# Performance work log

Hardware: AMD Instinct MI355X
Metric: run time of the kernel (lower is better)

Reference implementation:

```python
import jax, jax.numpy as jnp
import numpy as np
from jax import lax

DN = ('NCHW', 'OIHW', 'NCHW')
EPS = 1e-5

def conv2d(x, w):
    return lax.conv_general_dilated(x, w, (1, 1), 'VALID', dimension_numbers=DN)

def bn(x, g, b, m, v):
    # eval-mode BatchNorm2d, params shape [C]
    scale = (g / jnp.sqrt(v + EPS))[None, :, None, None]
    shift = (b - m * g / jnp.sqrt(v + EPS))[None, :, None, None]
    return x * scale + shift

def xcorr_depthwise(search, kernel):
    # search [B,C,Hs,Ws], kernel [B,C,hk,wk] -> [B,C,Hs-hk+1,Ws-wk+1]
    B, C, Hs, Ws = search.shape
    hk, wk = kernel.shape[2], kernel.shape[3]
    s = search.reshape(1, B * C, Hs, Ws)
    k = kernel.reshape(B * C, 1, hk, wk)
    out = lax.conv_general_dilated(s, k, (1, 1), 'VALID',
                                   dimension_numbers=DN,
                                   feature_group_count=B * C)
    return out.reshape(B, C, Hs - hk + 1, Ws - wk + 1)

def _bn_params(key, c):
    k1, k2, k3, k4 = jax.random.split(key, 4)
    g = jax.random.uniform(k1, (c,), jnp.float32, 0.5, 1.5)
    b = jax.random.normal(k2, (c,), jnp.float32) * 0.1
    m = jax.random.normal(k3, (c,), jnp.float32) * 0.1
    v = jax.random.uniform(k4, (c,), jnp.float32, 0.5, 1.5)
    return g, b, m, v

def setup_inputs() -> dict:
    key = jax.random.key(0)
    ks = jax.random.split(key, 10)
    IN, H, OUT = 256, 256, 10
    kernel = jax.random.normal(ks[0], (128, IN, 7, 7), jnp.float32)
    search = jax.random.normal(ks[1], (128, IN, 31, 31), jnp.float32)
    w_ck = jax.random.normal(ks[2], (H, IN, 3, 3), jnp.float32) * 0.05
    g1, b1, m1, v1 = _bn_params(ks[3], H)
    w_cs = jax.random.normal(ks[4], (H, IN, 3, 3), jnp.float32) * 0.05
    g2, b2, m2, v2 = _bn_params(ks[5], H)
    w_h1 = jax.random.normal(ks[6], (H, H, 1, 1), jnp.float32) * 0.05
    g3, b3, m3, v3 = _bn_params(ks[7], H)
    w_h2 = jax.random.normal(ks[8], (OUT, H, 1, 1), jnp.float32) * 0.05
    b_h2 = jax.random.normal(ks[9], (OUT,), jnp.float32) * 0.05
    return dict(kernel=kernel, search=search, w_ck=w_ck, g1=g1, b1=b1, m1=m1, v1=v1,
                w_cs=w_cs, g2=g2, b2=b2, m2=m2, v2=v2,
                w_h1=w_h1, g3=g3, b3=b3, m3=m3, v3=v3, w_h2=w_h2, b_h2=b_h2)

def reference(kernel, search, w_ck, g1, b1, m1, v1, w_cs, g2, b2, m2, v2,
              w_h1, g3, b3, m3, v3, w_h2, b_h2):
    # conv_kernel / conv_search branches: Conv3x3 -> BN -> ReLU
    k = jax.nn.relu(bn(conv2d(kernel, w_ck), g1, b1, m1, v1))   # [B,256,5,5]
    s = jax.nn.relu(bn(conv2d(search, w_cs), g2, b2, m2, v2))   # [B,256,29,29]
    # depthwise cross-correlation (search_crop/search_pos are None -> kernel_t = kernel)
    feat = xcorr_depthwise(s, k)                                 # [B,256,25,25]
    # head: Conv1x1 -> BN -> ReLU -> Conv1x1(+bias)
    h = jax.nn.relu(bn(conv2d(feat, w_h1), g3, b3, m3, v3))
    out = conv2d(h, w_h2) + b_h2[None, :, None, None]            # [B,10,25,25]
    return out
```

## Files before the change

kernel.cpp:

```cpp
#include <hip/hip_runtime.h>
#include <hip/hip_bf16.h>

#define EPS 1e-5f

typedef __attribute__((ext_vector_type(8))) short bf16x8;
typedef __attribute__((ext_vector_type(4))) float f32x4;
typedef __attribute__((ext_vector_type(4))) unsigned short u16x4;
typedef __attribute__((ext_vector_type(8))) unsigned short u16x8;

#define WAITVM8 asm volatile("s_waitcnt vmcnt(8)" ::: "memory")
#define WAITVM4 asm volatile("s_waitcnt vmcnt(4)" ::: "memory")
#define WAITVM0 asm volatile("s_waitcnt vmcnt(0)" ::: "memory")
#define BAR()   __builtin_amdgcn_s_barrier()

__device__ __forceinline__ void gld_lds16(const void* g, void* l) {
    __builtin_amdgcn_global_load_lds(
        (const __attribute__((address_space(1))) unsigned int*)g,
        (__attribute__((address_space(3))) unsigned int*)l, 16, 0, 0);
}

#define RD8(RA, RB, SEL) do {                                                  \
    const int _b = (SEL) * 8192;                                               \
    _Pragma("unroll") for (int _i = 0; _i < 4; ++_i)                           \
        RA[_i] = *reinterpret_cast<const bf16x8*>(&lA[_b + aoff + _i * 512]);  \
    _Pragma("unroll") for (int _j = 0; _j < 4; ++_j)                           \
        RB[_j] = *reinterpret_cast<const bf16x8*>(&lB[_b + boff + _j * 512]);  \
} while (0)

#define RD4(RA4, SEL) do {                                                     \
    const int _b = (SEL) * 8192;                                               \
    _Pragma("unroll") for (int _i = 0; _i < 4; ++_i)                           \
        RA4[_i] = *reinterpret_cast<const bf16x8*>(                            \
            &lA[_b + aoff + (_i + 4) * 512]);                                  \
} while (0)

#define MFQ(RA, RB, I0) do {                                                   \
    _Pragma("unroll") for (int _i = 0; _i < 4; ++_i)                           \
    _Pragma("unroll") for (int _j = 0; _j < 4; ++_j)                           \
        acc[(I0) + _i][_j] = __builtin_amdgcn_mfma_f32_16x16x32_bf16(          \
            RA[_i], RB[_j], acc[(I0) + _i][_j], 0, 0, 0);                      \
} while (0)

#define STEP(CA0, CA4, CB, NA0, NB, SELT, STAGE_STMT, WAIT_STMT, DORD) do {    \
    RD4(CA4, (SELT));                                                          \
    STAGE_STMT;                                                                \
    __builtin_amdgcn_s_setprio(1); MFQ(CA0, CB, 0);                            \
    __builtin_amdgcn_s_setprio(0);                                             \
    WAIT_STMT;                                                                 \
    BAR();                                                                     \
    if (DORD) RD8(NA0, NB, ((SELT) + 1) & 3);                                  \
    __builtin_amdgcn_s_setprio(1); MFQ(CA4, CB, 4);                            \
    __builtin_amdgcn_s_setprio(0);                                             \
} while (0)

template<int HIN, int WIN, int NTOT>
__device__ __forceinline__ void conv_dev(
    int bid, int tid,
    __hip_bfloat16* lA, __hip_bfloat16* lB,
    const __hip_bfloat16* __restrict__ xt,
    const __hip_bfloat16* __restrict__ wt,
    const float* __restrict__ g, const float* __restrict__ bb,
    const float* __restrict__ mm_, const float* __restrict__ vv,
    __hip_bfloat16* __restrict__ y)
{
    constexpr int HOUT = HIN - 2, WOUT = WIN - 2, POUT = HOUT * WOUT;
    const int n0  = bid * 256;
    const int wid = tid >> 6, lane = tid & 63;
    const int wr = wid >> 2, wc = wid & 3;

    const int arow = tid >> 2;
    const int seg  = (tid & 3) ^ ((tid >> 3) & 3);

    const size_t wbase0 = (size_t)arow * 2304 + seg * 8;
    const size_t wbase1 = (size_t)(arow + 128) * 2304 + seg * 8;

    int nr0 = n0 + arow;       if (nr0 > NTOT - 1) nr0 = NTOT - 1;
    int nr1 = n0 + arow + 128; if (nr1 > NTOT - 1) nr1 = NTOT - 1;
    int b0 = nr0 / POUT, p0 = nr0 % POUT, oy0 = p0 / WOUT, ox0 = p0 % WOUT;
    int b1 = nr1 / POUT, p1 = nr1 % POUT, oy1 = p1 / WOUT, ox1 = p1 % WOUT;
    const size_t xbase0 = (((size_t)b0 * HIN + oy0) * WIN + ox0) * 256 + seg * 8;
    const size_t xbase1 = (((size_t)b1 * HIN + oy1) * WIN + ox1) * 256 + seg * 8;

    auto stage = [&](int c0, int j, int sel) {
        char* a0 = (char*)lA + sel * 16384 + wid * 1024;
        char* b0p = (char*)lB + sel * 16384 + wid * 1024;
        const int woff = j * 256 + c0;
        gld_lds16(wt + wbase0 + woff, a0);
        gld_lds16(wt + wbase1 + woff, a0 + 8192);
        const int xoff = ((j / 3) * WIN + (j % 3)) * 256 + c0;
        gld_lds16(xt + xbase0 + xoff, b0p);
        gld_lds16(xt + xbase1 + xoff, b0p + 8192);
    };

    f32x4 acc[8][4];
#pragma unroll
    for (int i = 0; i < 8; ++i)
#pragma unroll
        for (int j = 0; j < 4; ++j)
            acc[i][j] = f32x4{0.f, 0.f, 0.f, 0.f};

    const int l15 = lane & 15, l16 = lane >> 4;
    const int slot = l16 ^ ((l15 >> 1) & 3);
    const int aoff = (wr * 128 + l15) * 32 + slot * 8;
    const int boff = (wc * 64  + l15) * 32 + slot * 8;

    bf16x8 pA0[4], pA4[4], pB[4], qA0[4], qA4[4], qB[4];

    stage(0, 0, 0); stage(0, 1, 1); stage(0, 2, 2);
    int js = 3, c0s = 0;
    WAITVM8; BAR();
    RD8(pA0, pB, 0);

#define ADVC do { ++js; if (js == 9) { js = 0; c0s += 32; } } while (0)
    for (int tt = 0; tt < 17; ++tt) {
        STEP(pA0, pA4, pB, qA0, qB, 0, stage(c0s, js, 3), WAITVM8, true); ADVC;
        STEP(qA0, qA4, qB, pA0, pB, 1, stage(c0s, js, 0), WAITVM8, true); ADVC;
        STEP(pA0, pA4, pB, qA0, qB, 2, stage(c0s, js, 1), WAITVM8, true); ADVC;
        STEP(qA0, qA4, qB, pA0, pB, 3, stage(c0s, js, 2), WAITVM8, true); ADVC;
    }
    STEP(pA0, pA4, pB, qA0, qB, 0, stage(c0s, js, 3), WAITVM8, true);
    STEP(qA0, qA4, qB, pA0, pB, 1, (void)0,           WAITVM4, true);
    STEP(pA0, pA4, pB, qA0, qB, 2, (void)0,           WAITVM0, true);
    STEP(qA0, qA4, qB, pA0, pB, 3, (void)0,           (void)0, false);
#undef ADVC

#pragma unroll
    for (int i = 0; i < 8; ++i) {
        const int co_b = wr * 128 + i * 16 + l16 * 4;
        float sc[4], sh[4];
#pragma unroll
        for (int r = 0; r < 4; ++r) {
            sc[r] = g[co_b + r] * rsqrtf(vv[co_b + r] + EPS);
            sh[r] = bb[co_b + r] - mm_[co_b + r] * sc[r];
        }
#pragma unroll
        for (int jj = 0; jj < 4; ++jj) {
            const int n = n0 + wc * 64 + jj * 16 + l15;
            if (n < NTOT) {
                u16x4 o;
#pragma unroll
                for (int r = 0; r < 4; ++r) {
                    const float v = fmaxf(fmaf(acc[i][jj][r], sc[r], sh[r]), 0.f);
                    __hip_bfloat16 hv = __float2bfloat16(v);
                    o[r] = *reinterpret_cast<unsigned short*>(&hv);
                }
                *reinterpret_cast<u16x4*>(&y[(size_t)n * 256 + co_b]) = o;
            }
        }
    }
}

__global__ __launch_bounds__(512, 2) void conv_both(
    const __hip_bfloat16* __restrict__ xt_s, const __hip_bfloat16* __restrict__ wt_cs,
    const float* __restrict__ g2, const float* __restrict__ b2,
    const float* __restrict__ m2, const float* __restrict__ v2,
    __hip_bfloat16* __restrict__ y2,
    const __hip_bfloat16* __restrict__ xt_k, const __hip_bfloat16* __restrict__ wt_ck,
    const float* __restrict__ g1, const float* __restrict__ b1,
    const float* __restrict__ m1, const float* __restrict__ v1,
    __hip_bfloat16* __restrict__ y1)
{
    __shared__ __align__(16) __hip_bfloat16 lA[4 * 8192];
    __shared__ __align__(16) __hip_bfloat16 lB[4 * 8192];
    if (blockIdx.x < 421)
        conv_dev<31, 31, 107648>(blockIdx.x, threadIdx.x, lA, lB,
                                 xt_s, wt_cs, g2, b2, m2, v2, y2);
    else
        conv_dev<7, 7, 3200>(blockIdx.x - 421, threadIdx.x, lA, lB,
                             xt_k, wt_ck, g1, b1, m1, v1, y1);
}

__device__ __forceinline__ void nhwc_body(
    const float* __restrict__ x, __hip_bfloat16* __restrict__ xt, int P,
    int bx, int b, float* t )
{
    const int p0 = bx * 32;
    const float* xb = x + (size_t)b * 256 * P;
    const int pl = threadIdx.x & 31, cg = threadIdx.x >> 5;
#pragma unroll
    for (int it = 0; it < 32; ++it) {
        int c = cg + it * 8, p = p0 + pl;
        t[c * 33 + pl] = (p < P) ? xb[(size_t)c * P + p] : 0.f;
    }
    __syncthreads();
    const int p = threadIdx.x >> 3, l8 = threadIdx.x & 7;
    if (p0 + p < P) {
        __hip_bfloat16* xo = xt + ((size_t)b * P + p0 + p) * 256;
#pragma unroll
        for (int j = 0; j < 4; ++j) {
            const int c0 = j * 64 + l8 * 8;
            u16x8 o;
#pragma unroll
            for (int r = 0; r < 8; ++r) {
                __hip_bfloat16 hv = __float2bfloat16(t[(c0 + r) * 33 + p]);
                o[r] = *reinterpret_cast<unsigned short*>(&hv);
            }
            *reinterpret_cast<u16x8*>(&xo[c0]) = o;
        }
    }
}

__global__ __launch_bounds__(256) void prepass(
    const float* __restrict__ w_ck, __hip_bfloat16* __restrict__ wt_ck,
    const float* __restrict__ w_cs, __hip_bfloat16* __restrict__ wt_cs,
    const float* __restrict__ w_h1, __hip_bfloat16* __restrict__ wh1,
    const float* __restrict__ kernel, __hip_bfloat16* __restrict__ xt_k,
    const float* __restrict__ search, __hip_bfloat16* __restrict__ xt_s)
{
    __shared__ float t[256 * 33];
    const int bid = blockIdx.x;
    if (bid < 512) {
        const float* w = (bid < 256) ? w_ck : w_cs;
        __hip_bfloat16* wt = (bid < 256) ? wt_ck : wt_cs;
        const int co = bid & 255, ci = threadIdx.x;
        const float* wp = w + (size_t)co * 2304 + (size_t)ci * 9;
        __hip_bfloat16* wo = wt + (size_t)co * 2304 + ci;
#pragma unroll
        for (int j = 0; j < 9; ++j)
            wo[(size_t)j * 256] = __float2bfloat16(wp[j]);
    } else if (bid < 768) {
        const int i = (bid - 512) * 256 + threadIdx.x;
        wh1[i] = __float2bfloat16(w_h1[i]);
    } else if (bid < 1024) {
        const int idx = bid - 768;
        nhwc_body(kernel, xt_k, 49, idx & 1, idx >> 1, t);
    } else {
        const int idx = bid - 1024;
        nhwc_body(search, xt_s, 961, idx % 31, idx / 31, t);
    }
}

__global__ __launch_bounds__(128) void xcorr_dw_nhwc2(
    const __hip_bfloat16* __restrict__ s,
    const __hip_bfloat16* __restrict__ k,
    __hip_bfloat16* __restrict__ f)
{
    const int py = blockIdx.x, b = blockIdx.y, c2 = threadIdx.x;
    const ushort2* sp = reinterpret_cast<const ushort2*>(s + (size_t)b * 841 * 256) + c2;
    const ushort2* kp = reinterpret_cast<const ushort2*>(k + (size_t)b * 25 * 256) + c2;

    float a0[25], a1[25];
#pragma unroll
    for (int i = 0; i < 25; ++i) { a0[i] = 0.f; a1[i] = 0.f; }

    for (int ky = 0; ky < 5; ++ky) {
        const ushort2* srp = sp + (size_t)(py + ky) * 29 * 128;
        float s0[29], s1[29];
#pragma unroll
        for (int rx = 0; rx < 29; ++rx) {
            ushort2 u = srp[(size_t)rx * 128];
            unsigned int w0 = (unsigned int)u.x << 16, w1 = (unsigned int)u.y << 16;
            s0[rx] = *reinterpret_cast<float*>(&w0);
            s1[rx] = *reinterpret_cast<float*>(&w1);
        }
#pragma unroll
        for (int kx = 0; kx < 5; ++kx) {
            ushort2 u = kp[(size_t)(ky * 5 + kx) * 128];
            unsigned int w0 = (unsigned int)u.x << 16, w1 = (unsigned int)u.y << 16;
            const float k0 = *reinterpret_cast<float*>(&w0);
            const float k1 = *reinterpret_cast<float*>(&w1);
#pragma unroll
            for (int px = 0; px < 25; ++px) {
                a0[px] = fmaf(s0[px + kx], k0, a0[px]);
                a1[px] = fmaf(s1[px + kx], k1, a1[px]);
            }
        }
    }

    ushort2* fp = reinterpret_cast<ushort2*>(f + ((size_t)b * 625 + (size_t)py * 25) * 256) + c2;
#pragma unroll
    for (int px = 0; px < 25; ++px) {
        __hip_bfloat16 h0 = __float2bfloat16(a0[px]);
        __hip_bfloat16 h1 = __float2bfloat16(a1[px]);
        ushort2 o;
        o.x = *reinterpret_cast<unsigned short*>(&h0);
        o.y = *reinterpret_cast<unsigned short*>(&h1);
        fp[(size_t)px * 128] = o;
    }
}

__global__ __launch_bounds__(512) void head_fused8(
    const __hip_bfloat16* __restrict__ f,
    const __hip_bfloat16* __restrict__ w1,
    const float* __restrict__ g, const float* __restrict__ bb,
    const float* __restrict__ mm_, const float* __restrict__ vv,
    const float* __restrict__ w2,
    const float* __restrict__ b2v,
    float* __restrict__ out)
{
    constexpr int NTOT = 80000;
    const int n0  = blockIdx.x * 256;
    const int tid = threadIdx.x;
    const int wid = tid >> 6, lane = tid & 63;
    const int wr = wid >> 2, wc = wid & 3;

    __shared__ __align__(16) __hip_bfloat16 lA[4 * 8192];
    __shared__ __align__(16) __hip_bfloat16 lB[4 * 8192];

    const int arow = tid >> 2;
    const int seg  = (tid & 3) ^ ((tid >> 3) & 3);

    const size_t wbase0 = (size_t)arow * 256 + seg * 8;
    const size_t wbase1 = (size_t)(arow + 128) * 256 + seg * 8;
    int nr0 = n0 + arow;       if (nr0 > NTOT - 1) nr0 = NTOT - 1;
    int nr1 = n0 + arow + 128; if (nr1 > NTOT - 1) nr1 = NTOT - 1;
    const size_t xbase0 = (size_t)nr0 * 256 + seg * 8;
    const size_t xbase1 = (size_t)nr1 * 256 + seg * 8;

    auto stage = [&](int c0, int sel) {
        char* a0 = (char*)lA + sel * 16384 + wid * 1024;
        char* b0p = (char*)lB + sel * 16384 + wid * 1024;
        gld_lds16(w1 + wbase0 + c0, a0);
        gld_lds16(w1 + wbase1 + c0, a0 + 8192);
        gld_lds16(f + xbase0 + c0, b0p);
        gld_lds16(f + xbase1 + c0, b0p + 8192);
    };

    f32x4 acc[8][4];
#pragma unroll
    for (int i = 0; i < 8; ++i)
#pragma unroll
        for (int j = 0; j < 4; ++j)
            acc[i][j] = f32x4{0.f, 0.f, 0.f, 0.f};

    const int l15 = lane & 15, l16 = lane >> 4;
    const int slot = l16 ^ ((l15 >> 1) & 3);
    const int aoff = (wr * 128 + l15) * 32 + slot * 8;
    const int boff = (wc * 64  + l15) * 32 + slot * 8;

    bf16x8 pA0[4], pA4[4], pB[4], qA0[4], qA4[4], qB[4];

    stage(0, 0); stage(32, 1); stage(64, 2);
    WAITVM8; BAR();
    RD8(pA0, pB, 0);

    STEP(pA0, pA4, pB, qA0, qB, 0, stage(96, 3),  WAITVM8, true);
    STEP(qA0, qA4, qB, pA0, pB, 1, stage(128, 0), WAITVM8, true);
    STEP(pA0, pA4, pB, qA0, qB, 2, stage(160, 1), WAITVM8, true);
    STEP(qA0, qA4, qB, pA0, pB, 3, stage(192, 2), WAITVM8, true);
    STEP(pA0, pA4, pB, qA0, qB, 0, stage(224, 3), WAITVM8, true);
    STEP(qA0, qA4, qB, pA0, pB, 1, (void)0,       WAITVM4, true);
    STEP(pA0, pA4, pB, qA0, qB, 2, (void)0,       WAITVM0, true);
    STEP(qA0, qA4, qB, pA0, pB, 3, (void)0,       (void)0, false);

    __syncthreads();
    float* lw   = (float*)lA;
    float* lred = (float*)lB;
    for (int t = tid; t < 2560; t += 512) lw[t] = w2[t];
    if (tid < 10) lw[2560 + tid] = b2v[tid];
    __syncthreads();

    float p[4][10];
#pragma unroll
    for (int jj = 0; jj < 4; ++jj)
#pragma unroll
        for (int o = 0; o < 10; ++o) p[jj][o] = 0.f;

#pragma unroll
    for (int i = 0; i < 8; ++i) {
        const int co_b = wr * 128 + i * 16 + l16 * 4;
        float sc[4], sh[4];
#pragma unroll
        for (int r = 0; r < 4; ++r) {
            sc[r] = g[co_b + r] * rsqrtf(vv[co_b + r] + EPS);
            sh[r] = bb[co_b + r] - mm_[co_b + r] * sc[r];
        }
        float w4[10][4];
#pragma unroll
        for (int o = 0; o < 10; ++o) {
            f32x4 wv = *reinterpret_cast<const f32x4*>(&lw[o * 256 + co_b]);
#pragma unroll
            for (int r = 0; r < 4; ++r) w4[o][r] = wv[r];
        }
#pragma unroll
        for (int jj = 0; jj < 4; ++jj) {
            float hv[4];
#pragma unroll
            for (int r = 0; r < 4; ++r)
                hv[r] = fmaxf(fmaf(acc[i][jj][r], sc[r], sh[r]), 0.f);
#pragma unroll
            for (int o = 0; o < 10; ++o)
#pragma unroll
                for (int r = 0; r < 4; ++r)
                    p[jj][o] = fmaf(hv[r], w4[o][r], p[jj][o]);
        }
    }

#pragma unroll
    for (int jj = 0; jj < 4; ++jj)
#pragma unroll
        for (int o = 0; o < 10; ++o) {
            float v = p[jj][o];
            v += __shfl_xor(v, 16, 64);
            v += __shfl_xor(v, 32, 64);
            p[jj][o] = v;
        }

    if (wr == 0 && l16 == 0) {
#pragma unroll
        for (int jj = 0; jj < 4; ++jj)
#pragma unroll
            for (int o = 0; o < 10; ++o)
                lred[((wc * 4 + jj) * 16 + l15) * 10 + o] = p[jj][o];
    }
    __syncthreads();
    if (wr == 1) {
#pragma unroll
        for (int jj = 0; jj < 4; ++jj) {
            const int n = n0 + wc * 64 + jj * 16 + l15;
            if (n < NTOT) {
                const int bi = n / 625, pp = n % 625;
#pragma unroll
                for (int t = 0; t < 3; ++t) {
                    const int o = l16 + 4 * t;
                    if (o < 10) {
                        float v = p[jj][o]
                                + lred[((wc * 4 + jj) * 16 + l15) * 10 + o]
                                + lw[2560 + o];
                        out[((size_t)bi * 10 + o) * 625 + pp] = v;
                    }
                }
            }
        }
    }
}

extern "C" void kernel_launch(void* const* d_in, const int* in_sizes, int n_in,
                              void* d_out, int out_size, void* d_ws, size_t ws_size,
                              hipStream_t stream) {
    const float* kernel = (const float*)d_in[0];
    const float* search = (const float*)d_in[1];
    const float* w_ck   = (const float*)d_in[2];
    const float* g1 = (const float*)d_in[3];
    const float* b1 = (const float*)d_in[4];
    const float* m1 = (const float*)d_in[5];
    const float* v1 = (const float*)d_in[6];
    const float* w_cs   = (const float*)d_in[7];
    const float* g2 = (const float*)d_in[8];
    const float* b2 = (const float*)d_in[9];
    const float* m2 = (const float*)d_in[10];
    const float* v2 = (const float*)d_in[11];
    const float* w_h1   = (const float*)d_in[12];
    const float* g3 = (const float*)d_in[13];
    const float* b3 = (const float*)d_in[14];
    const float* m3 = (const float*)d_in[15];
    const float* v3 = (const float*)d_in[16];
    const float* w_h2   = (const float*)d_in[17];
    const float* b_h2   = (const float*)d_in[18];

    float* out = (float*)d_out;

    __hip_bfloat16* ws = (__hip_bfloat16*)d_ws;
    __hip_bfloat16* y1    = ws;
    __hip_bfloat16* y2    = ws + (size_t)819200;
    __hip_bfloat16* wt_ck = ws + (size_t)28377088;
    __hip_bfloat16* wt_cs = ws + (size_t)28966912;
    __hip_bfloat16* wh1   = ws + (size_t)29556736;
    __hip_bfloat16* xt_k  = ws + (size_t)29622272;
    __hip_bfloat16* xt_s  = ws + (size_t)31227904;
    __hip_bfloat16* feat  = ws + (size_t)29622272;

    (void)in_sizes; (void)n_in; (void)out_size; (void)ws_size;

    prepass<<<4992, 256, 0, stream>>>(w_ck, wt_ck, w_cs, wt_cs, w_h1, wh1,
                                      kernel, xt_k, search, xt_s);

    conv_both<<<434, 512, 0, stream>>>(xt_s, wt_cs, g2, b2, m2, v2, y2,
                                       xt_k, wt_ck, g1, b1, m1, v1, y1);

    xcorr_dw_nhwc2<<<dim3(25, 128), 128, 0, stream>>>(y2, y1, feat);

    head_fused8<<<313, 512, 0, stream>>>(feat, wh1, g3, b3, m3, v3, w_h2, b_h2, out);
}
```

Before: 315.2 us.

## Compute five output rows per thread in depthwise xcorr to reuse search rows

The depthwise cross-correlation now gives each thread one channel and a strip of five output rows. Each of the nine search rows is loaded once and applied to all output rows it touches, and the 25 kernel taps stay in registers. Before, each block handled a single output row for two channels and reloaded five search rows per output row. This cuts redundant global loads about 2.8x, but needs 125 accumulators plus 29 row values per thread, so register pressure and occupancy may suffer. The grid also shrinks to 640 blocks of 256 threads, and loads and stores are now 16-bit per thread instead of paired.

```diff
diff --git a/kernel.cpp b/kernel.cpp
--- a/kernel.cpp
+++ b/kernel.cpp
@@ -230,52 +230,55 @@
     }
 }
 
-__global__ __launch_bounds__(128) void xcorr_dw_nhwc2(
+__global__ __launch_bounds__(256) void xcorr_strip(
     const __hip_bfloat16* __restrict__ s,
     const __hip_bfloat16* __restrict__ k,
     __hip_bfloat16* __restrict__ f)
 {
-    const int py = blockIdx.x, b = blockIdx.y, c2 = threadIdx.x;
-    const ushort2* sp = reinterpret_cast<const ushort2*>(s + (size_t)b * 841 * 256) + c2;
-    const ushort2* kp = reinterpret_cast<const ushort2*>(k + (size_t)b * 25 * 256) + c2;
-
-    float a0[25], a1[25];
-#pragma unroll
-    for (int i = 0; i < 25; ++i) { a0[i] = 0.f; a1[i] = 0.f; }
-
-    for (int ky = 0; ky < 5; ++ky) {
-        const ushort2* srp = sp + (size_t)(py + ky) * 29 * 128;
-        float s0[29], s1[29];
-#pragma unroll
-        for (int rx = 0; rx < 29; ++rx) {
-            ushort2 u = srp[(size_t)rx * 128];
-            unsigned int w0 = (unsigned int)u.x << 16, w1 = (unsigned int)u.y << 16;
-            s0[rx] = *reinterpret_cast<float*>(&w0);
-            s1[rx] = *reinterpret_cast<float*>(&w1);
-        }
-#pragma unroll
-        for (int kx = 0; kx < 5; ++kx) {
-            ushort2 u = kp[(size_t)(ky * 5 + kx) * 128];
-            unsigned int w0 = (unsigned int)u.x << 16, w1 = (unsigned int)u.y << 16;
-            const float k0 = *reinterpret_cast<float*>(&w0);
-            const float k1 = *reinterpret_cast<float*>(&w1);
-#pragma unroll
-            for (int px = 0; px < 25; ++px) {
-                a0[px] = fmaf(s0[px + kx], k0, a0[px]);
-                a1[px] = fmaf(s1[px + kx], k1, a1[px]);
+    const int st = blockIdx.x, b = blockIdx.y, c = threadIdx.x;
+    const int py0 = st * 5;
+    const __hip_bfloat16* sp = s + (size_t)b * 841 * 256 + c;
+    const __hip_bfloat16* kp = k + (size_t)b * 25 * 256 + c;
+
+    float kv[25];
+#pragma unroll
+    for (int i = 0; i < 25; ++i)
+        kv[i] = __bfloat162float(kp[(size_t)i * 256]);
+
+    float acc[5][25];
+#pragma unroll
+    for (int p = 0; p < 5; ++p)
+#pragma unroll
+        for (int px = 0; px < 25; ++px) acc[p][px] = 0.f;
+
+#pragma unroll
+    for (int r = 0; r < 9; ++r) {
+        float srow[29];
+        const __hip_bfloat16* srp = sp + (size_t)(py0 + r) * 29 * 256;
+#pragma unroll
+        for (int rx = 0; rx < 29; ++rx)
+            srow[rx] = __bfloat162float(srp[(size_t)rx * 256]);
+#pragma unroll
+        for (int p = 0; p < 5; ++p) {
+            if (r >= p && r - p <= 4) {
+                const int ky = r - p;
+#pragma unroll
+                for (int kx = 0; kx < 5; ++kx) {
+                    const float kvv = kv[ky * 5 + kx];
+#pragma unroll
+                    for (int px = 0; px < 25; ++px)
+                        acc[p][px] = fmaf(srow[px + kx], kvv, acc[p][px]);
+                }
             }
         }
     }
 
-    ushort2* fp = reinterpret_cast<ushort2*>(f + ((size_t)b * 625 + (size_t)py * 25) * 256) + c2;
-#pragma unroll
-    for (int px = 0; px < 25; ++px) {
-        __hip_bfloat16 h0 = __float2bfloat16(a0[px]);
-        __hip_bfloat16 h1 = __float2bfloat16(a1[px]);
-        ushort2 o;
-        o.x = *reinterpret_cast<unsigned short*>(&h0);
-        o.y = *reinterpret_cast<unsigned short*>(&h1);
-        fp[(size_t)px * 128] = o;
+#pragma unroll
+    for (int p = 0; p < 5; ++p) {
+        __hip_bfloat16* fp = f + ((size_t)b * 625 + (size_t)(py0 + p) * 25) * 256 + c;
+#pragma unroll
+        for (int px = 0; px < 25; ++px)
+            fp[(size_t)px * 256] = __float2bfloat16(acc[p][px]);
     }
 }
 
@@ -468,7 +471,7 @@
     conv_both<<<434, 512, 0, stream>>>(xt_s, wt_cs, g2, b2, m2, v2, y2,
                                        xt_k, wt_ck, g1, b1, m1, v1, y1);
 
-    xcorr_dw_nhwc2<<<dim3(25, 128), 128, 0, stream>>>(y2, y1, feat);
+    xcorr_strip<<<dim3(5, 128), 256, 0, stream>>>(y2, y1, feat);
 
     head_fused8<<<313, 512, 0, stream>>>(feat, wh1, g3, b3, m3, v3, w_h2, b_h2, out);
 }
```

New measurement: 302.1 us. 1.04x faster.
